# Optimization experiments

Hardware: AMD Instinct MI355X
Metric: run time of the kernel (lower is better)

Reference implementation:

```python
import jax, jax.numpy as jnp
import numpy as np


def setup_inputs() -> dict:
    key = jax.random.key(0)
    kq, kk = jax.random.split(key)
    B, Q, K, D = 32, 512, 512, 1024
    queries = jax.random.normal(kq, (B, Q, D), dtype=jnp.float32)
    keys = jax.random.normal(kk, (B, K, D), dtype=jnp.float32)
    # ProbabilityConverter learned scalars (is_temperature=True, is_bias=True)
    temperature = jnp.ones((), dtype=jnp.float32)
    bias = jnp.zeros((), dtype=jnp.float32)
    return {"queries": queries, "keys": keys, "temperature": temperature, "bias": bias}


def reference(queries, keys, temperature, bias):
    # Dot scoring: (B, Q, D) x (B, K, D) -> (B, Q, K)
    logits = jnp.einsum("bqd,bkd->bqk", queries, keys)
    # keys.eq(0.0)[:, :, :1].transpose(1, 2): mask positions where first key feature == 0
    key_mask = (keys[:, :, 0] == 0.0)[:, None, :]  # (B, 1, K)
    neg_inf = jnp.array(-jnp.inf, dtype=logits.dtype)
    logits = jnp.where(key_mask, neg_inf, logits)
    # confidence = sigmoid((logsumexp(logits) + bias) * temperature)
    approx_max_logit = jax.nn.logsumexp(logits, axis=-1)  # (B, Q)
    confidence = jax.nn.sigmoid((approx_max_logit + bias) * temperature)
    attn = jax.nn.softmax(logits, axis=-1)  # (B, Q, K)
    return attn, confidence
```

## Files before the change

kernel.cpp:

```cpp
#include <hip/hip_runtime.h>
#include <math.h>
#include <stdint.h>


#define NB 32
#define NQ 512
#define NK 512
#define ND 1024
#define BK 32
#define NT (ND / BK)
#define BM1 64
#define BM8 64
#define ASTRIDE 520
#define TILE_BYTES 65536
#define WS_TILES ((size_t)NB * NT * TILE_BYTES)
#define WS_TOTAL (WS_TILES + (size_t)NB * NK * 4)

typedef __attribute__((ext_vector_type(8))) short short8;
typedef __attribute__((ext_vector_type(4))) float f32x4;

__device__ __forceinline__ void bf_split(float x, unsigned& hbits, float& lo) {
  unsigned u = __float_as_uint(x);
  unsigned r = u + 0x7fffu + ((u >> 16) & 1u);
  hbits = r & 0xffff0000u;
  lo = x - __uint_as_float(hbits);
}
__device__ __forceinline__ unsigned pack_rn(float x0, float x1) {
  unsigned u0 = __float_as_uint(x0), u1 = __float_as_uint(x1);
  unsigned r0 = u0 + 0x7fffu + ((u0 >> 16) & 1u);
  unsigned r1 = u1 + 0x7fffu + ((u1 >> 16) & 1u);
  return (r0 >> 16) | (r1 & 0xffff0000u);
}

__device__ __forceinline__ int lds_off_write(int r, int c4) {
  int slot = ((c4 >> 1) + (r >> 1)) & 3;
  return r * 32 + slot * 8 + (c4 & 1) * 4;
}
__device__ __forceinline__ int lds_off_read(int r, int quad) {
  int slot = (quad + (r >> 1)) & 3;
  return r * 32 + slot * 8;
}

__global__ __launch_bounds__(256)
void convert_k(const float* __restrict__ Kg, unsigned char* __restrict__ ws) {
  const int bx = blockIdx.x;
  const int batch = bx >> 5, kt = bx & 31;
  const float* src = Kg + (size_t)batch * NK * ND + kt * BK;
  unsigned short* hiB = (unsigned short*)(ws + (size_t)bx * TILE_BYTES);
  unsigned short* loB = hiB + 32768 / 2;
  float* maskB = (float*)(ws + WS_TILES) + batch * NK;

#pragma unroll
  for (int i = 0; i < 16; ++i) {
    int idx = threadIdx.x + 256 * i;
    int c = idx >> 3, c4 = idx & 7;
    float4 v = *(const float4*)(src + (size_t)c * ND + c4 * 4);
    unsigned h0, h1, h2, h3;
    float l0, l1, l2, l3;
    bf_split(v.x, h0, l0); bf_split(v.y, h1, l1);
    bf_split(v.z, h2, l2); bf_split(v.w, h3, l3);
    int off = c * 32 + c4 * 4;
    *(uint2*)(&hiB[off]) = make_uint2((h0 >> 16) | h1, (h2 >> 16) | h3);
    *(uint2*)(&loB[off]) = make_uint2(pack_rn(l0, l1), pack_rn(l2, l3));
    if (kt == 0 && c4 == 0) maskB[c] = v.x;
  }
}

#define MFMA_BF16 __builtin_amdgcn_mfma_f32_16x16x32_bf16

#define BODY8(KT, CURB, NXTB)                                                  \
  do {                                                                         \
    if ((KT) + 1 < NT) {                                                       \
      const unsigned char* tb = wsB + (size_t)((KT) + 1) * TILE_BYTES;         \
      NXTB[0] = *(const short8*)(tb + boff);                                   \
      NXTB[1] = *(const short8*)(tb + 1024 + boff);                            \
      NXTB[2] = *(const short8*)(tb + 32768 + boff);                           \
      NXTB[3] = *(const short8*)(tb + 32768 + 1024 + boff);                    \
    }                                                                          \
    const int ktL = (KT) & 15;                                                 \
    short8 ahi[4], alo[4];                                                     \
    _Pragma("unroll") for (int mt = 0; mt < 4; ++mt) {                         \
      int off = (mt * 16 + ln15) * ASTRIDE + ktL * 32 + quad * 8;              \
      ahi[mt] = *(const short8*)(&sAhi[off]);                                  \
      alo[mt] = *(const short8*)(&sAlo[off]);                                  \
    }                                                                          \
    _Pragma("unroll") for (int nt = 0; nt < 2; ++nt) {                         \
      _Pragma("unroll") for (int mt = 0; mt < 4; ++mt) {                       \
        acc[mt][nt] = MFMA_BF16(ahi[mt], CURB[nt], acc[mt][nt], 0, 0, 0);      \
        acc[mt][nt] = MFMA_BF16(ahi[mt], CURB[2 + nt], acc[mt][nt], 0, 0, 0);  \
        acc[mt][nt] = MFMA_BF16(alo[mt], CURB[nt], acc[mt][nt], 0, 0, 0);      \
      }                                                                        \
    }                                                                          \
  } while (0)

__global__ __launch_bounds__(1024, 4)
void attn_fused_v8(const float* __restrict__ Qg,
                   const unsigned char* __restrict__ ws,
                   const float* __restrict__ Tp, const float* __restrict__ Bp,
                   float* __restrict__ attn, float* __restrict__ conf) {
  __shared__ __align__(16) unsigned short sAhi[BM8 * ASTRIDE];
  __shared__ __align__(16) unsigned short sAlo[BM8 * ASTRIDE];
  __shared__ __align__(16) float sRedA[BM8][16];
  __shared__ __align__(16) float sRedB[BM8][16];

  const int tid = threadIdx.x;
  const int g = blockIdx.x;
  const int batch = g & 31;
  const int q0 = (g >> 5) * BM8;
  const int ln = tid & 63, w = tid >> 6;
  const int ln15 = ln & 15, quad = ln >> 4;
  const int col0 = w * 32;

  const float* Qp = Qg + ((size_t)batch * NQ + q0) * ND;
  const unsigned char* wsB = ws + (size_t)batch * NT * TILE_BYTES;
  const float* maskB = (const float*)(ws + WS_TILES) + batch * NK;

  const int boff = (col0 << 6) + (ln15 << 6) + (quad << 4);

  f32x4 acc[4][2];
#pragma unroll
  for (int mt = 0; mt < 4; ++mt)
#pragma unroll
    for (int nt = 0; nt < 2; ++nt) acc[mt][nt] = (f32x4){0.f, 0.f, 0.f, 0.f};

  auto stage_half = [&](int h) {
#pragma unroll
    for (int i = 0; i < 4; ++i) {
      int idx = tid + 1024 * i;
      int row = idx >> 6, kc8 = idx & 63;
      const float* p = Qp + (size_t)row * ND + h * 512 + kc8 * 8;
      float4 va = *(const float4*)(p);
      float4 vb = *(const float4*)(p + 4);
      unsigned h0, h1, h2, h3, h4, h5, h6, h7;
      float l0, l1, l2, l3, l4, l5, l6, l7;
      bf_split(va.x, h0, l0); bf_split(va.y, h1, l1);
      bf_split(va.z, h2, l2); bf_split(va.w, h3, l3);
      bf_split(vb.x, h4, l4); bf_split(vb.y, h5, l5);
      bf_split(vb.z, h6, l6); bf_split(vb.w, h7, l7);
      int off = row * ASTRIDE + kc8 * 8;
      *(uint4*)(&sAhi[off]) = make_uint4((h0 >> 16) | h1, (h2 >> 16) | h3,
                                         (h4 >> 16) | h5, (h6 >> 16) | h7);
      *(uint4*)(&sAlo[off]) = make_uint4(pack_rn(l0, l1), pack_rn(l2, l3),
                                         pack_rn(l4, l5), pack_rn(l6, l7));
    }
  };

  stage_half(0);
  short8 pbA[4], pbB[4];
  pbA[0] = *(const short8*)(wsB + boff);
  pbA[1] = *(const short8*)(wsB + 1024 + boff);
  pbA[2] = *(const short8*)(wsB + 32768 + boff);
  pbA[3] = *(const short8*)(wsB + 32768 + 1024 + boff);
  __syncthreads();

#pragma unroll 1
  for (int kt = 0; kt < 16; kt += 2) {
    BODY8(kt, pbA, pbB);
    BODY8(kt + 1, pbB, pbA);
  }

  __syncthreads();
  stage_half(1);
  __syncthreads();

#pragma unroll 1
  for (int kt = 16; kt < 32; kt += 2) {
    BODY8(kt, pbA, pbB);
    BODY8(kt + 1, pbB, pbA);
  }

  const float NEGINF = -__builtin_inff();
  float rm[4][4];
#pragma unroll
  for (int mt = 0; mt < 4; ++mt)
#pragma unroll
    for (int rg = 0; rg < 4; ++rg) rm[mt][rg] = NEGINF;

#pragma unroll
  for (int nt = 0; nt < 2; ++nt) {
    int col = col0 + nt * 16 + ln15;
    bool msk = (maskB[col] == 0.0f);
#pragma unroll
    for (int mt = 0; mt < 4; ++mt)
#pragma unroll
      for (int rg = 0; rg < 4; ++rg) {
        float v = msk ? NEGINF : acc[mt][nt][rg];
        acc[mt][nt][rg] = v;
        rm[mt][rg] = fmaxf(rm[mt][rg], v);
      }
  }
#pragma unroll
  for (int mt = 0; mt < 4; ++mt)
#pragma unroll
    for (int rg = 0; rg < 4; ++rg) {
      float v = rm[mt][rg];
#pragma unroll
      for (int d = 1; d < 16; d <<= 1) v = fmaxf(v, __shfl_xor(v, d, 64));
      rm[mt][rg] = v;
    }
  if (ln15 == 0) {
#pragma unroll
    for (int mt = 0; mt < 4; ++mt)
#pragma unroll
      for (int rg = 0; rg < 4; ++rg)
        sRedA[mt * 16 + quad * 4 + rg][w] = rm[mt][rg];
  }
  __syncthreads();

  float gmax[4][4], gsum[4][4];
#pragma unroll
  for (int mt = 0; mt < 4; ++mt)
#pragma unroll
    for (int rg = 0; rg < 4; ++rg) {
      int row = mt * 16 + quad * 4 + rg;
      f32x4 p0 = *(const f32x4*)(&sRedA[row][0]);
      f32x4 p1 = *(const f32x4*)(&sRedA[row][4]);
      f32x4 p2 = *(const f32x4*)(&sRedA[row][8]);
      f32x4 p3 = *(const f32x4*)(&sRedA[row][12]);
      float m01 = fmaxf(fmaxf(fmaxf(p0[0], p0[1]), fmaxf(p0[2], p0[3])),
                        fmaxf(fmaxf(p1[0], p1[1]), fmaxf(p1[2], p1[3])));
      float m23 = fmaxf(fmaxf(fmaxf(p2[0], p2[1]), fmaxf(p2[2], p2[3])),
                        fmaxf(fmaxf(p3[0], p3[1]), fmaxf(p3[2], p3[3])));
      gmax[mt][rg] = fmaxf(m01, m23);
      gsum[mt][rg] = 0.f;
    }

#pragma unroll
  for (int nt = 0; nt < 2; ++nt)
#pragma unroll
    for (int mt = 0; mt < 4; ++mt)
#pragma unroll
      for (int rg = 0; rg < 4; ++rg) {
        float e = __expf(acc[mt][nt][rg] - gmax[mt][rg]);
        acc[mt][nt][rg] = e;
        gsum[mt][rg] += e;
      }
#pragma unroll
  for (int mt = 0; mt < 4; ++mt)
#pragma unroll
    for (int rg = 0; rg < 4; ++rg) {
      float v = gsum[mt][rg];
#pragma unroll
      for (int d = 1; d < 16; d <<= 1) v += __shfl_xor(v, d, 64);
      gsum[mt][rg] = v;
    }
  if (ln15 == 0) {
#pragma unroll
    for (int mt = 0; mt < 4; ++mt)
#pragma unroll
      for (int rg = 0; rg < 4; ++rg)
        sRedB[mt * 16 + quad * 4 + rg][w] = gsum[mt][rg];
  }
  __syncthreads();
#pragma unroll
  for (int mt = 0; mt < 4; ++mt)
#pragma unroll
    for (int rg = 0; rg < 4; ++rg) {
      int row = mt * 16 + quad * 4 + rg;
      f32x4 p0 = *(const f32x4*)(&sRedB[row][0]);
      f32x4 p1 = *(const f32x4*)(&sRedB[row][4]);
      f32x4 p2 = *(const f32x4*)(&sRedB[row][8]);
      f32x4 p3 = *(const f32x4*)(&sRedB[row][12]);
      gsum[mt][rg] = ((p0[0] + p0[1]) + (p0[2] + p0[3])) +
                     ((p1[0] + p1[1]) + (p1[2] + p1[3])) +
                     ((p2[0] + p2[1]) + (p2[2] + p2[3])) +
                     ((p3[0] + p3[1]) + (p3[2] + p3[3]));
    }

  float* outBase = attn + ((size_t)batch * NQ + q0) * NK;
#pragma unroll
  for (int mt = 0; mt < 4; ++mt)
#pragma unroll
    for (int rg = 0; rg < 4; ++rg) {
      int row = mt * 16 + quad * 4 + rg;
      float inv = 1.0f / gsum[mt][rg];
#pragma unroll
      for (int nt = 0; nt < 2; ++nt)
        outBase[(size_t)row * NK + col0 + nt * 16 + ln15] = acc[mt][nt][rg] * inv;
    }

  if (w == 0 && ln15 == 0) {
    float tv = Tp[0], bv = Bp[0];
#pragma unroll
    for (int mt = 0; mt < 4; ++mt)
#pragma unroll
      for (int rg = 0; rg < 4; ++rg) {
        int row = mt * 16 + quad * 4 + rg;
        float lse = gmax[mt][rg] + __logf(gsum[mt][rg]);
        float t = (lse + bv) * tv;
        conf[(size_t)batch * NQ + q0 + row] = 1.0f / (1.0f + __expf(-t));
      }
  }
}

__global__ __launch_bounds__(256, 1)
void attn_fused_v1(const float* __restrict__ Qg, const float* __restrict__ Kg,
                   const float* __restrict__ Tp, const float* __restrict__ Bp,
                   float* __restrict__ attn, float* __restrict__ conf) {
  __shared__ __align__(16) unsigned short sAhi[BM1 * BK];
  __shared__ __align__(16) unsigned short sAlo[BM1 * BK];
  __shared__ __align__(16) unsigned short sBhi[NK * BK];
  __shared__ __align__(16) unsigned short sBlo[NK * BK];
  __shared__ float sRedA[4][BM1];
  __shared__ float sRedB[4][BM1];

  const int tid = threadIdx.x;
  const int g = blockIdx.x;
  const int batch = g & 31;
  const int q0 = (g >> 5) * BM1;
  const int ln = tid & 63, w = tid >> 6;
  const int ln15 = ln & 15, quad = ln >> 4;
  const int wn0 = w * 128;

  const float* Qp = Qg + ((size_t)batch * NQ + q0) * ND;
  const float* Kp = Kg + (size_t)batch * NK * ND;

  f32x4 acc[4][8];
#pragma unroll
  for (int mt = 0; mt < 4; ++mt)
#pragma unroll
    for (int nt = 0; nt < 8; ++nt) acc[mt][nt] = (f32x4){0.f, 0.f, 0.f, 0.f};

  float4 pb[16], pa[2];
#pragma unroll
  for (int i = 0; i < 16; ++i) {
    int idx = tid + 256 * i, r = idx >> 3, c4 = idx & 7;
    pb[i] = *(const float4*)(Kp + (size_t)r * ND + c4 * 4);
  }
#pragma unroll
  for (int i = 0; i < 2; ++i) {
    int idx = tid + 256 * i, r = idx >> 3, c4 = idx & 7;
    pa[i] = *(const float4*)(Qp + (size_t)r * ND + c4 * 4);
  }

  for (int kt = 0; kt < NT; ++kt) {
    if (kt) __syncthreads();
#pragma unroll
    for (int i = 0; i < 2; ++i) {
      int idx = tid + 256 * i, r = idx >> 3, c4 = idx & 7;
      int off = lds_off_write(r, c4);
      unsigned h0, h1, h2, h3; float l0, l1, l2, l3;
      bf_split(pa[i].x, h0, l0); bf_split(pa[i].y, h1, l1);
      bf_split(pa[i].z, h2, l2); bf_split(pa[i].w, h3, l3);
      *(uint2*)(&sAhi[off]) = make_uint2((h0 >> 16) | h1, (h2 >> 16) | h3);
      *(uint2*)(&sAlo[off]) = make_uint2(pack_rn(l0, l1), pack_rn(l2, l3));
    }
#pragma unroll
    for (int i = 0; i < 16; ++i) {
      int idx = tid + 256 * i, r = idx >> 3, c4 = idx & 7;
      int off = lds_off_write(r, c4);
      unsigned h0, h1, h2, h3; float l0, l1, l2, l3;
      bf_split(pb[i].x, h0, l0); bf_split(pb[i].y, h1, l1);
      bf_split(pb[i].z, h2, l2); bf_split(pb[i].w, h3, l3);
      *(uint2*)(&sBhi[off]) = make_uint2((h0 >> 16) | h1, (h2 >> 16) | h3);
      *(uint2*)(&sBlo[off]) = make_uint2(pack_rn(l0, l1), pack_rn(l2, l3));
    }
    __syncthreads();

    if (kt < NT - 1) {
      const float* Kq = Kp + (kt + 1) * BK;
      const float* Qq = Qp + (kt + 1) * BK;
#pragma unroll
      for (int i = 0; i < 16; ++i) {
        int idx = tid + 256 * i, r = idx >> 3, c4 = idx & 7;
        pb[i] = *(const float4*)(Kq + (size_t)r * ND + c4 * 4);
      }
#pragma unroll
      for (int i = 0; i < 2; ++i) {
        int idx = tid + 256 * i, r = idx >> 3, c4 = idx & 7;
        pa[i] = *(const float4*)(Qq + (size_t)r * ND + c4 * 4);
      }
    }

    short8 ahi[4], alo[4];
#pragma unroll
    for (int mt = 0; mt < 4; ++mt) {
      int off = lds_off_read(mt * 16 + ln15, quad);
      ahi[mt] = *(const short8*)(&sAhi[off]);
      alo[mt] = *(const short8*)(&sAlo[off]);
    }
#pragma unroll
    for (int nt = 0; nt < 8; ++nt) {
      int off = lds_off_read(wn0 + nt * 16 + ln15, quad);
      short8 bhi = *(const short8*)(&sBhi[off]);
      short8 blo = *(const short8*)(&sBlo[off]);
#pragma unroll
      for (int mt = 0; mt < 4; ++mt) {
        acc[mt][nt] = MFMA_BF16(ahi[mt], bhi, acc[mt][nt], 0, 0, 0);
        acc[mt][nt] = MFMA_BF16(ahi[mt], blo, acc[mt][nt], 0, 0, 0);
        acc[mt][nt] = MFMA_BF16(alo[mt], bhi, acc[mt][nt], 0, 0, 0);
      }
    }
  }

  const float NEGINF = -__builtin_inff();
  float rm[4][4];
#pragma unroll
  for (int mt = 0; mt < 4; ++mt)
#pragma unroll
    for (int rg = 0; rg < 4; ++rg) rm[mt][rg] = NEGINF;
#pragma unroll
  for (int nt = 0; nt < 8; ++nt) {
    int col = wn0 + nt * 16 + ln15;
    bool msk = (Kp[(size_t)col * ND] == 0.0f);
#pragma unroll
    for (int mt = 0; mt < 4; ++mt)
#pragma unroll
      for (int rg = 0; rg < 4; ++rg) {
        float v = msk ? NEGINF : acc[mt][nt][rg];
        acc[mt][nt][rg] = v;
        rm[mt][rg] = fmaxf(rm[mt][rg], v);
      }
  }
#pragma unroll
  for (int mt = 0; mt < 4; ++mt)
#pragma unroll
    for (int rg = 0; rg < 4; ++rg) {
      float v = rm[mt][rg];
#pragma unroll
      for (int d = 1; d < 16; d <<= 1) v = fmaxf(v, __shfl_xor(v, d, 64));
      rm[mt][rg] = v;
    }
  if (ln15 == 0)
#pragma unroll
    for (int mt = 0; mt < 4; ++mt)
#pragma unroll
      for (int rg = 0; rg < 4; ++rg)
        sRedA[w][mt * 16 + quad * 4 + rg] = rm[mt][rg];
  __syncthreads();

  float gmax[4][4], gsum[4][4];
#pragma unroll
  for (int mt = 0; mt < 4; ++mt)
#pragma unroll
    for (int rg = 0; rg < 4; ++rg) {
      int row = mt * 16 + quad * 4 + rg;
      gmax[mt][rg] = fmaxf(fmaxf(sRedA[0][row], sRedA[1][row]),
                           fmaxf(sRedA[2][row], sRedA[3][row]));
      gsum[mt][rg] = 0.f;
    }
#pragma unroll
  for (int nt = 0; nt < 8; ++nt)
#pragma unroll
    for (int mt = 0; mt < 4; ++mt)
#pragma unroll
      for (int rg = 0; rg < 4; ++rg) {
        float e = __expf(acc[mt][nt][rg] - gmax[mt][rg]);
        acc[mt][nt][rg] = e;
        gsum[mt][rg] += e;
      }
#pragma unroll
  for (int mt = 0; mt < 4; ++mt)
#pragma unroll
    for (int rg = 0; rg < 4; ++rg) {
      float v = gsum[mt][rg];
#pragma unroll
      for (int d = 1; d < 16; d <<= 1) v += __shfl_xor(v, d, 64);
      gsum[mt][rg] = v;
    }
  if (ln15 == 0)
#pragma unroll
    for (int mt = 0; mt < 4; ++mt)
#pragma unroll
      for (int rg = 0; rg < 4; ++rg)
        sRedB[w][mt * 16 + quad * 4 + rg] = gsum[mt][rg];
  __syncthreads();
#pragma unroll
  for (int mt = 0; mt < 4; ++mt)
#pragma unroll
    for (int rg = 0; rg < 4; ++rg) {
      int row = mt * 16 + quad * 4 + rg;
      gsum[mt][rg] = sRedB[0][row] + sRedB[1][row] + sRedB[2][row] + sRedB[3][row];
    }

  float* outBase = attn + ((size_t)batch * NQ + q0) * NK;
#pragma unroll
  for (int mt = 0; mt < 4; ++mt)
#pragma unroll
    for (int rg = 0; rg < 4; ++rg) {
      int row = mt * 16 + quad * 4 + rg;
      float inv = 1.0f / gsum[mt][rg];
#pragma unroll
      for (int nt = 0; nt < 8; ++nt)
        outBase[(size_t)row * NK + wn0 + nt * 16 + ln15] = acc[mt][nt][rg] * inv;
    }
  if (w == 0 && ln15 == 0) {
    float tv = Tp[0], bv = Bp[0];
#pragma unroll
    for (int mt = 0; mt < 4; ++mt)
#pragma unroll
      for (int rg = 0; rg < 4; ++rg) {
        int row = mt * 16 + quad * 4 + rg;
        float lse = gmax[mt][rg] + __logf(gsum[mt][rg]);
        float t = (lse + bv) * tv;
        conf[(size_t)batch * NQ + q0 + row] = 1.0f / (1.0f + __expf(-t));
      }
  }
}

extern "C" void kernel_launch(void* const* d_in, const int* in_sizes, int n_in,
                              void* d_out, int out_size, void* d_ws, size_t ws_size,
                              hipStream_t stream) {
  const float* q = (const float*)d_in[0];
  const float* k = (const float*)d_in[1];
  const float* temp = (const float*)d_in[2];
  const float* bias = (const float*)d_in[3];
  float* attn = (float*)d_out;
  float* conf = attn + (size_t)NB * NQ * NK;

  if (ws_size >= WS_TOTAL) {
    hipLaunchKernelGGL(convert_k, dim3(NB * NT), dim3(256), 0, stream,
                       k, (unsigned char*)d_ws);
    hipLaunchKernelGGL(attn_fused_v8, dim3(NB * (NQ / BM8)), dim3(1024), 0, stream,
                       q, (const unsigned char*)d_ws, temp, bias, attn, conf);
  } else {
    hipLaunchKernelGGL(attn_fused_v1, dim3(NB * (NQ / BM1)), dim3(256), 0, stream,
                       q, k, temp, bias, attn, conf);
  }
}
```

Before: 218.6 us.

## Fuse K bf16 hi/lo split into main attention kernel, drop convert pass

Removes the separate kernel that pre-split K into bf16 hi/lo tiles in workspace. The fused kernel now loads fp32 K rows directly into registers and splits them in-register before the MFMAs, and reads the mask from K. This eliminates a launch and the workspace write/read round trip. In exchange, every Q-tile block repeats the split arithmetic on K. The small-workspace fallback kernel is deleted.

```diff
diff --git a/kernel.cpp b/kernel.cpp
--- a/kernel.cpp
+++ b/kernel.cpp
@@ -9,15 +9,12 @@
 #define ND 1024
 #define BK 32
 #define NT (ND / BK)
-#define BM1 64
-#define BM8 64
+#define BM9 64
 #define ASTRIDE 520
-#define TILE_BYTES 65536
-#define WS_TILES ((size_t)NB * NT * TILE_BYTES)
-#define WS_TOTAL (WS_TILES + (size_t)NB * NK * 4)
 
 typedef __attribute__((ext_vector_type(8))) short short8;
 typedef __attribute__((ext_vector_type(4))) float f32x4;
+typedef __attribute__((ext_vector_type(4))) unsigned int uint32x4;
 
 __device__ __forceinline__ void bf_split(float x, unsigned& hbits, float& lo) {
   unsigned u = __float_as_uint(x);
@@ -32,50 +29,33 @@
   return (r0 >> 16) | (r1 & 0xffff0000u);
 }
 
-__device__ __forceinline__ int lds_off_write(int r, int c4) {
-  int slot = ((c4 >> 1) + (r >> 1)) & 3;
-  return r * 32 + slot * 8 + (c4 & 1) * 4;
-}
-__device__ __forceinline__ int lds_off_read(int r, int quad) {
-  int slot = (quad + (r >> 1)) & 3;
-  return r * 32 + slot * 8;
-}
-
-__global__ __launch_bounds__(256)
-void convert_k(const float* __restrict__ Kg, unsigned char* __restrict__ ws) {
-  const int bx = blockIdx.x;
-  const int batch = bx >> 5, kt = bx & 31;
-  const float* src = Kg + (size_t)batch * NK * ND + kt * BK;
-  unsigned short* hiB = (unsigned short*)(ws + (size_t)bx * TILE_BYTES);
-  unsigned short* loB = hiB + 32768 / 2;
-  float* maskB = (float*)(ws + WS_TILES) + batch * NK;
-
-#pragma unroll
-  for (int i = 0; i < 16; ++i) {
-    int idx = threadIdx.x + 256 * i;
-    int c = idx >> 3, c4 = idx & 7;
-    float4 v = *(const float4*)(src + (size_t)c * ND + c4 * 4);
-    unsigned h0, h1, h2, h3;
-    float l0, l1, l2, l3;
-    bf_split(v.x, h0, l0); bf_split(v.y, h1, l1);
-    bf_split(v.z, h2, l2); bf_split(v.w, h3, l3);
-    int off = c * 32 + c4 * 4;
-    *(uint2*)(&hiB[off]) = make_uint2((h0 >> 16) | h1, (h2 >> 16) | h3);
-    *(uint2*)(&loB[off]) = make_uint2(pack_rn(l0, l1), pack_rn(l2, l3));
-    if (kt == 0 && c4 == 0) maskB[c] = v.x;
-  }
+__device__ __forceinline__ void split8(const float4& va, const float4& vb,
+                                       short8& hi, short8& lo) {
+  unsigned h0, h1, h2, h3, h4, h5, h6, h7;
+  float l0, l1, l2, l3, l4, l5, l6, l7;
+  bf_split(va.x, h0, l0); bf_split(va.y, h1, l1);
+  bf_split(va.z, h2, l2); bf_split(va.w, h3, l3);
+  bf_split(vb.x, h4, l4); bf_split(vb.y, h5, l5);
+  bf_split(vb.z, h6, l6); bf_split(vb.w, h7, l7);
+  uint32x4 hu = {(h0 >> 16) | h1, (h2 >> 16) | h3,
+                 (h4 >> 16) | h5, (h6 >> 16) | h7};
+  uint32x4 lu = {pack_rn(l0, l1), pack_rn(l2, l3),
+                 pack_rn(l4, l5), pack_rn(l6, l7)};
+  hi = __builtin_bit_cast(short8, hu);
+  lo = __builtin_bit_cast(short8, lu);
 }
 
 #define MFMA_BF16 __builtin_amdgcn_mfma_f32_16x16x32_bf16
 
-#define BODY8(KT, CURB, NXTB)                                                  \
+#define BODY9(KT, CURR, NXTR)                                                  \
   do {                                                                         \
     if ((KT) + 1 < NT) {                                                       \
-      const unsigned char* tb = wsB + (size_t)((KT) + 1) * TILE_BYTES;         \
-      NXTB[0] = *(const short8*)(tb + boff);                                   \
-      NXTB[1] = *(const short8*)(tb + 1024 + boff);                            \
-      NXTB[2] = *(const short8*)(tb + 32768 + boff);                           \
-      NXTB[3] = *(const short8*)(tb + 32768 + 1024 + boff);                    \
+      const float* kp0 = kb0 + ((KT) + 1) * BK;                                \
+      const float* kp1 = kb1 + ((KT) + 1) * BK;                                \
+      NXTR[0] = *(const float4*)(kp0);                                         \
+      NXTR[1] = *(const float4*)(kp0 + 4);                                     \
+      NXTR[2] = *(const float4*)(kp1);                                         \
+      NXTR[3] = *(const float4*)(kp1 + 4);                                     \
     }                                                                          \
     const int ktL = (KT) & 15;                                                 \
     short8 ahi[4], alo[4];                                                     \
@@ -84,38 +64,41 @@
       ahi[mt] = *(const short8*)(&sAhi[off]);                                  \
       alo[mt] = *(const short8*)(&sAlo[off]);                                  \
     }                                                                          \
-    _Pragma("unroll") for (int nt = 0; nt < 2; ++nt) {                         \
-      _Pragma("unroll") for (int mt = 0; mt < 4; ++mt) {                       \
-        acc[mt][nt] = MFMA_BF16(ahi[mt], CURB[nt], acc[mt][nt], 0, 0, 0);      \
-        acc[mt][nt] = MFMA_BF16(ahi[mt], CURB[2 + nt], acc[mt][nt], 0, 0, 0);  \
-        acc[mt][nt] = MFMA_BF16(alo[mt], CURB[nt], acc[mt][nt], 0, 0, 0);      \
-      }                                                                        \
+    short8 bhi0, blo0, bhi1, blo1;                                             \
+    split8(CURR[0], CURR[1], bhi0, blo0);                                      \
+    split8(CURR[2], CURR[3], bhi1, blo1);                                      \
+    _Pragma("unroll") for (int mt = 0; mt < 4; ++mt) {                         \
+      acc[mt][0] = MFMA_BF16(ahi[mt], bhi0, acc[mt][0], 0, 0, 0);              \
+      acc[mt][0] = MFMA_BF16(ahi[mt], blo0, acc[mt][0], 0, 0, 0);              \
+      acc[mt][0] = MFMA_BF16(alo[mt], bhi0, acc[mt][0], 0, 0, 0);              \
+      acc[mt][1] = MFMA_BF16(ahi[mt], bhi1, acc[mt][1], 0, 0, 0);              \
+      acc[mt][1] = MFMA_BF16(ahi[mt], blo1, acc[mt][1], 0, 0, 0);              \
+      acc[mt][1] = MFMA_BF16(alo[mt], bhi1, acc[mt][1], 0, 0, 0);              \
     }                                                                          \
   } while (0)
 
 __global__ __launch_bounds__(1024, 4)
-void attn_fused_v8(const float* __restrict__ Qg,
-                   const unsigned char* __restrict__ ws,
+void attn_fused_v9(const float* __restrict__ Qg, const float* __restrict__ Kg,
                    const float* __restrict__ Tp, const float* __restrict__ Bp,
                    float* __restrict__ attn, float* __restrict__ conf) {
-  __shared__ __align__(16) unsigned short sAhi[BM8 * ASTRIDE];
-  __shared__ __align__(16) unsigned short sAlo[BM8 * ASTRIDE];
-  __shared__ __align__(16) float sRedA[BM8][16];
-  __shared__ __align__(16) float sRedB[BM8][16];
+  __shared__ __align__(16) unsigned short sAhi[BM9 * ASTRIDE];
+  __shared__ __align__(16) unsigned short sAlo[BM9 * ASTRIDE];
+  __shared__ __align__(16) float sRedA[BM9][16];
+  __shared__ __align__(16) float sRedB[BM9][16];
 
   const int tid = threadIdx.x;
   const int g = blockIdx.x;
   const int batch = g & 31;
-  const int q0 = (g >> 5) * BM8;
+  const int q0 = (g >> 5) * BM9;
   const int ln = tid & 63, w = tid >> 6;
   const int ln15 = ln & 15, quad = ln >> 4;
   const int col0 = w * 32;
 
   const float* Qp = Qg + ((size_t)batch * NQ + q0) * ND;
-  const unsigned char* wsB = ws + (size_t)batch * NT * TILE_BYTES;
-  const float* maskB = (const float*)(ws + WS_TILES) + batch * NK;
-
-  const int boff = (col0 << 6) + (ln15 << 6) + (quad << 4);
+  const float* Kp = Kg + (size_t)batch * NK * ND;
+
+  const float* kb0 = Kp + (size_t)(col0 + ln15) * ND + quad * 8;
+  const float* kb1 = kb0 + 16 * ND;
 
   f32x4 acc[4][2];
 #pragma unroll
@@ -146,17 +129,17 @@
   };
 
   stage_half(0);
-  short8 pbA[4], pbB[4];
-  pbA[0] = *(const short8*)(wsB + boff);
-  pbA[1] = *(const short8*)(wsB + 1024 + boff);
-  pbA[2] = *(const short8*)(wsB + 32768 + boff);
-  pbA[3] = *(const short8*)(wsB + 32768 + 1024 + boff);
+  float4 pbA[4], pbB[4];
+  pbA[0] = *(const float4*)(kb0);
+  pbA[1] = *(const float4*)(kb0 + 4);
+  pbA[2] = *(const float4*)(kb1);
+  pbA[3] = *(const float4*)(kb1 + 4);
   __syncthreads();
 
 #pragma unroll 1
   for (int kt = 0; kt < 16; kt += 2) {
-    BODY8(kt, pbA, pbB);
-    BODY8(kt + 1, pbB, pbA);
+    BODY9(kt, pbA, pbB);
+    BODY9(kt + 1, pbB, pbA);
   }
 
   __syncthreads();
@@ -165,8 +148,8 @@
 
 #pragma unroll 1
   for (int kt = 16; kt < 32; kt += 2) {
-    BODY8(kt, pbA, pbB);
-    BODY8(kt + 1, pbB, pbA);
+    BODY9(kt, pbA, pbB);
+    BODY9(kt + 1, pbB, pbA);
   }
 
   const float NEGINF = -__builtin_inff();
@@ -179,7 +162,7 @@
 #pragma unroll
   for (int nt = 0; nt < 2; ++nt) {
     int col = col0 + nt * 16 + ln15;
-    bool msk = (maskB[col] == 0.0f);
+    bool msk = (Kp[(size_t)col * ND] == 0.0f);
 #pragma unroll
     for (int mt = 0; mt < 4; ++mt)
 #pragma unroll
@@ -293,211 +276,6 @@
   }
 }
 
-__global__ __launch_bounds__(256, 1)
-void attn_fused_v1(const float* __restrict__ Qg, const float* __restrict__ Kg,
-                   const float* __restrict__ Tp, const float* __restrict__ Bp,
-                   float* __restrict__ attn, float* __restrict__ conf) {
-  __shared__ __align__(16) unsigned short sAhi[BM1 * BK];
-  __shared__ __align__(16) unsigned short sAlo[BM1 * BK];
-  __shared__ __align__(16) unsigned short sBhi[NK * BK];
-  __shared__ __align__(16) unsigned short sBlo[NK * BK];
-  __shared__ float sRedA[4][BM1];
-  __shared__ float sRedB[4][BM1];
-
-  const int tid = threadIdx.x;
-  const int g = blockIdx.x;
-  const int batch = g & 31;
-  const int q0 = (g >> 5) * BM1;
-  const int ln = tid & 63, w = tid >> 6;
-  const int ln15 = ln & 15, quad = ln >> 4;
-  const int wn0 = w * 128;
-
-  const float* Qp = Qg + ((size_t)batch * NQ + q0) * ND;
-  const float* Kp = Kg + (size_t)batch * NK * ND;
-
-  f32x4 acc[4][8];
-#pragma unroll
-  for (int mt = 0; mt < 4; ++mt)
-#pragma unroll
-    for (int nt = 0; nt < 8; ++nt) acc[mt][nt] = (f32x4){0.f, 0.f, 0.f, 0.f};
-
-  float4 pb[16], pa[2];
-#pragma unroll
-  for (int i = 0; i < 16; ++i) {
-    int idx = tid + 256 * i, r = idx >> 3, c4 = idx & 7;
-    pb[i] = *(const float4*)(Kp + (size_t)r * ND + c4 * 4);
-  }
-#pragma unroll
-  for (int i = 0; i < 2; ++i) {
-    int idx = tid + 256 * i, r = idx >> 3, c4 = idx & 7;
-    pa[i] = *(const float4*)(Qp + (size_t)r * ND + c4 * 4);
-  }
-
-  for (int kt = 0; kt < NT; ++kt) {
-    if (kt) __syncthreads();
-#pragma unroll
-    for (int i = 0; i < 2; ++i) {
-      int idx = tid + 256 * i, r = idx >> 3, c4 = idx & 7;
-      int off = lds_off_write(r, c4);
-      unsigned h0, h1, h2, h3; float l0, l1, l2, l3;
-      bf_split(pa[i].x, h0, l0); bf_split(pa[i].y, h1, l1);
-      bf_split(pa[i].z, h2, l2); bf_split(pa[i].w, h3, l3);
-      *(uint2*)(&sAhi[off]) = make_uint2((h0 >> 16) | h1, (h2 >> 16) | h3);
-      *(uint2*)(&sAlo[off]) = make_uint2(pack_rn(l0, l1), pack_rn(l2, l3));
-    }
-#pragma unroll
-    for (int i = 0; i < 16; ++i) {
-      int idx = tid + 256 * i, r = idx >> 3, c4 = idx & 7;
-      int off = lds_off_write(r, c4);
-      unsigned h0, h1, h2, h3; float l0, l1, l2, l3;
-      bf_split(pb[i].x, h0, l0); bf_split(pb[i].y, h1, l1);
-      bf_split(pb[i].z, h2, l2); bf_split(pb[i].w, h3, l3);
-      *(uint2*)(&sBhi[off]) = make_uint2((h0 >> 16) | h1, (h2 >> 16) | h3);
-      *(uint2*)(&sBlo[off]) = make_uint2(pack_rn(l0, l1), pack_rn(l2, l3));
-    }
-    __syncthreads();
-
-    if (kt < NT - 1) {
-      const float* Kq = Kp + (kt + 1) * BK;
-      const float* Qq = Qp + (kt + 1) * BK;
-#pragma unroll
-      for (int i = 0; i < 16; ++i) {
-        int idx = tid + 256 * i, r = idx >> 3, c4 = idx & 7;
-        pb[i] = *(const float4*)(Kq + (size_t)r * ND + c4 * 4);
-      }
-#pragma unroll
-      for (int i = 0; i < 2; ++i) {
-        int idx = tid + 256 * i, r = idx >> 3, c4 = idx & 7;
-        pa[i] = *(const float4*)(Qq + (size_t)r * ND + c4 * 4);
-      }
-    }
-
-    short8 ahi[4], alo[4];
-#pragma unroll
-    for (int mt = 0; mt < 4; ++mt) {
-      int off = lds_off_read(mt * 16 + ln15, quad);
-      ahi[mt] = *(const short8*)(&sAhi[off]);
-      alo[mt] = *(const short8*)(&sAlo[off]);
-    }
-#pragma unroll
-    for (int nt = 0; nt < 8; ++nt) {
-      int off = lds_off_read(wn0 + nt * 16 + ln15, quad);
-      short8 bhi = *(const short8*)(&sBhi[off]);
-      short8 blo = *(const short8*)(&sBlo[off]);
-#pragma unroll
-      for (int mt = 0; mt < 4; ++mt) {
-        acc[mt][nt] = MFMA_BF16(ahi[mt], bhi, acc[mt][nt], 0, 0, 0);
-        acc[mt][nt] = MFMA_BF16(ahi[mt], blo, acc[mt][nt], 0, 0, 0);
-        acc[mt][nt] = MFMA_BF16(alo[mt], bhi, acc[mt][nt], 0, 0, 0);
-      }
-    }
-  }
-
-  const float NEGINF = -__builtin_inff();
-  float rm[4][4];
-#pragma unroll
-  for (int mt = 0; mt < 4; ++mt)
-#pragma unroll
-    for (int rg = 0; rg < 4; ++rg) rm[mt][rg] = NEGINF;
-#pragma unroll
-  for (int nt = 0; nt < 8; ++nt) {
-    int col = wn0 + nt * 16 + ln15;
-    bool msk = (Kp[(size_t)col * ND] == 0.0f);
-#pragma unroll
-    for (int mt = 0; mt < 4; ++mt)
-#pragma unroll
-      for (int rg = 0; rg < 4; ++rg) {
-        float v = msk ? NEGINF : acc[mt][nt][rg];
-        acc[mt][nt][rg] = v;
-        rm[mt][rg] = fmaxf(rm[mt][rg], v);
-      }
-  }
-#pragma unroll
-  for (int mt = 0; mt < 4; ++mt)
-#pragma unroll
-    for (int rg = 0; rg < 4; ++rg) {
-      float v = rm[mt][rg];
-#pragma unroll
-      for (int d = 1; d < 16; d <<= 1) v = fmaxf(v, __shfl_xor(v, d, 64));
-      rm[mt][rg] = v;
-    }
-  if (ln15 == 0)
-#pragma unroll
-    for (int mt = 0; mt < 4; ++mt)
-#pragma unroll
-      for (int rg = 0; rg < 4; ++rg)
-        sRedA[w][mt * 16 + quad * 4 + rg] = rm[mt][rg];
-  __syncthreads();
-
-  float gmax[4][4], gsum[4][4];
-#pragma unroll
-  for (int mt = 0; mt < 4; ++mt)
-#pragma unroll
-    for (int rg = 0; rg < 4; ++rg) {
-      int row = mt * 16 + quad * 4 + rg;
-      gmax[mt][rg] = fmaxf(fmaxf(sRedA[0][row], sRedA[1][row]),
-                           fmaxf(sRedA[2][row], sRedA[3][row]));
-      gsum[mt][rg] = 0.f;
-    }
-#pragma unroll
-  for (int nt = 0; nt < 8; ++nt)
-#pragma unroll
-    for (int mt = 0; mt < 4; ++mt)
-#pragma unroll
-      for (int rg = 0; rg < 4; ++rg) {
-        float e = __expf(acc[mt][nt][rg] - gmax[mt][rg]);
-        acc[mt][nt][rg] = e;
-        gsum[mt][rg] += e;
-      }
-#pragma unroll
-  for (int mt = 0; mt < 4; ++mt)
-#pragma unroll
-    for (int rg = 0; rg < 4; ++rg) {
-      float v = gsum[mt][rg];
-#pragma unroll
-      for (int d = 1; d < 16; d <<= 1) v += __shfl_xor(v, d, 64);
-      gsum[mt][rg] = v;
-    }
-  if (ln15 == 0)
-#pragma unroll
-    for (int mt = 0; mt < 4; ++mt)
-#pragma unroll
-      for (int rg = 0; rg < 4; ++rg)
-        sRedB[w][mt * 16 + quad * 4 + rg] = gsum[mt][rg];
-  __syncthreads();
-#pragma unroll
-  for (int mt = 0; mt < 4; ++mt)
-#pragma unroll
-    for (int rg = 0; rg < 4; ++rg) {
-      int row = mt * 16 + quad * 4 + rg;
-      gsum[mt][rg] = sRedB[0][row] + sRedB[1][row] + sRedB[2][row] + sRedB[3][row];
-    }
-
-  float* outBase = attn + ((size_t)batch * NQ + q0) * NK;
-#pragma unroll
-  for (int mt = 0; mt < 4; ++mt)
-#pragma unroll
-    for (int rg = 0; rg < 4; ++rg) {
-      int row = mt * 16 + quad * 4 + rg;
-      float inv = 1.0f / gsum[mt][rg];
-#pragma unroll
-      for (int nt = 0; nt < 8; ++nt)
-        outBase[(size_t)row * NK + wn0 + nt * 16 + ln15] = acc[mt][nt][rg] * inv;
-    }
-  if (w == 0 && ln15 == 0) {
-    float tv = Tp[0], bv = Bp[0];
-#pragma unroll
-    for (int mt = 0; mt < 4; ++mt)
-#pragma unroll
-      for (int rg = 0; rg < 4; ++rg) {
-        int row = mt * 16 + quad * 4 + rg;
-        float lse = gmax[mt][rg] + __logf(gsum[mt][rg]);
-        float t = (lse + bv) * tv;
-        conf[(size_t)batch * NQ + q0 + row] = 1.0f / (1.0f + __expf(-t));
-      }
-  }
-}
-
 extern "C" void kernel_launch(void* const* d_in, const int* in_sizes, int n_in,
                               void* d_out, int out_size, void* d_ws, size_t ws_size,
                               hipStream_t stream) {
@@ -508,13 +286,7 @@
   float* attn = (float*)d_out;
   float* conf = attn + (size_t)NB * NQ * NK;
 
-  if (ws_size >= WS_TOTAL) {
-    hipLaunchKernelGGL(convert_k, dim3(NB * NT), dim3(256), 0, stream,
-                       k, (unsigned char*)d_ws);
-    hipLaunchKernelGGL(attn_fused_v8, dim3(NB * (NQ / BM8)), dim3(1024), 0, stream,
-                       q, (const unsigned char*)d_ws, temp, bias, attn, conf);
-  } else {
-    hipLaunchKernelGGL(attn_fused_v1, dim3(NB * (NQ / BM1)), dim3(256), 0, stream,
-                       q, k, temp, bias, attn, conf);
-  }
-}
+  (void)d_ws; (void)ws_size;
+  hipLaunchKernelGGL(attn_fused_v9, dim3(NB * (NQ / BM9)), dim3(1024), 0, stream,
+                     q, k, temp, bias, attn, conf);
+}
```

Measured after the change: 221.6 us. No clear change (+1.4%).

## Split key dimension across blocks with partial softmax and separate combine pass

Applied to the files above, without the earlier changes.

The fused kernel is replaced by a partial kernel where each block covers 128 query rows and half of the keys. It stages Q in four K-quarters and adds a barrier after each MFMA step. Each block writes unnormalized exponentials plus per-half row max and sum to workspace. A new combine kernel then rescales every attention row and computes confidence. The aim is to reuse the key tiles across more query rows and reduce per-block LDS, at the cost of an extra full read and write of the attention output and one more launch.

```diff
diff --git a/kernel.cpp b/kernel.cpp
--- a/kernel.cpp
+++ b/kernel.cpp
@@ -10,11 +10,14 @@
 #define BK 32
 #define NT (ND / BK)
 #define BM1 64
-#define BM8 64
-#define ASTRIDE 520
+#define BMP 128
+#define KHALF 256
+#define AST2 264
 #define TILE_BYTES 65536
 #define WS_TILES ((size_t)NB * NT * TILE_BYTES)
-#define WS_TOTAL (WS_TILES + (size_t)NB * NK * 4)
+#define MASK_BYTES ((size_t)NB * NK * 4)
+#define MS_BYTES ((size_t)NB * NQ * 2 * 4)
+#define WS_TOTAL (WS_TILES + MASK_BYTES + 2 * MS_BYTES)
 
 typedef __attribute__((ext_vector_type(8))) short short8;
 typedef __attribute__((ext_vector_type(4))) float f32x4;
@@ -68,7 +71,7 @@
 
 #define MFMA_BF16 __builtin_amdgcn_mfma_f32_16x16x32_bf16
 
-#define BODY8(KT, CURB, NXTB)                                                  \
+#define BODYP(KT, CURB, NXTB)                                                  \
   do {                                                                         \
     if ((KT) + 1 < NT) {                                                       \
       const unsigned char* tb = wsB + (size_t)((KT) + 1) * TILE_BYTES;         \
@@ -77,10 +80,10 @@
       NXTB[2] = *(const short8*)(tb + 32768 + boff);                           \
       NXTB[3] = *(const short8*)(tb + 32768 + 1024 + boff);                    \
     }                                                                          \
-    const int ktL = (KT) & 15;                                                 \
+    const int ktL = (KT) & 7;                                                  \
     short8 ahi[4], alo[4];                                                     \
     _Pragma("unroll") for (int mt = 0; mt < 4; ++mt) {                         \
-      int off = (mt * 16 + ln15) * ASTRIDE + ktL * 32 + quad * 8;              \
+      int off = (wr * 64 + mt * 16 + ln15) * AST2 + ktL * 32 + quad * 8;       \
       ahi[mt] = *(const short8*)(&sAhi[off]);                                  \
       alo[mt] = *(const short8*)(&sAlo[off]);                                  \
     }                                                                          \
@@ -91,31 +94,33 @@
         acc[mt][nt] = MFMA_BF16(alo[mt], CURB[nt], acc[mt][nt], 0, 0, 0);      \
       }                                                                        \
     }                                                                          \
+    __builtin_amdgcn_s_barrier();                                              \
   } while (0)
 
 __global__ __launch_bounds__(1024, 4)
-void attn_fused_v8(const float* __restrict__ Qg,
-                   const unsigned char* __restrict__ ws,
-                   const float* __restrict__ Tp, const float* __restrict__ Bp,
-                   float* __restrict__ attn, float* __restrict__ conf) {
-  __shared__ __align__(16) unsigned short sAhi[BM8 * ASTRIDE];
-  __shared__ __align__(16) unsigned short sAlo[BM8 * ASTRIDE];
-  __shared__ __align__(16) float sRedA[BM8][16];
-  __shared__ __align__(16) float sRedB[BM8][16];
+void attn_part(const float* __restrict__ Qg, const unsigned char* __restrict__ ws,
+               float* __restrict__ attn, float* __restrict__ Mws,
+               float* __restrict__ Sws) {
+  __shared__ __align__(16) unsigned short sAhi[BMP * AST2];
+  __shared__ __align__(16) unsigned short sAlo[BMP * AST2];
+  __shared__ __align__(16) float sRed[BMP][8];
 
   const int tid = threadIdx.x;
   const int g = blockIdx.x;
-  const int batch = g & 31;
-  const int q0 = (g >> 5) * BM8;
+  const int b = g & 31;
+  const int qh = g >> 5;
+  const int qc = qh >> 1;
+  const int h = qh & 1;
   const int ln = tid & 63, w = tid >> 6;
   const int ln15 = ln & 15, quad = ln >> 4;
-  const int col0 = w * 32;
-
-  const float* Qp = Qg + ((size_t)batch * NQ + q0) * ND;
-  const unsigned char* wsB = ws + (size_t)batch * NT * TILE_BYTES;
-  const float* maskB = (const float*)(ws + WS_TILES) + batch * NK;
-
-  const int boff = (col0 << 6) + (ln15 << 6) + (quad << 4);
+  const int wr = w >> 3, wc = w & 7;
+  const int col0 = wc * 32;
+
+  const float* Qp = Qg + ((size_t)b * NQ + qc * BMP) * ND;
+  const unsigned char* wsB = ws + (size_t)b * NT * TILE_BYTES;
+  const float* maskB = (const float*)(ws + WS_TILES) + b * NK;
+
+  const int boff = ((h * KHALF + col0 + ln15) << 6) + (quad << 4);
 
   f32x4 acc[4][2];
 #pragma unroll
@@ -123,12 +128,12 @@
 #pragma unroll
     for (int nt = 0; nt < 2; ++nt) acc[mt][nt] = (f32x4){0.f, 0.f, 0.f, 0.f};
 
-  auto stage_half = [&](int h) {
+  auto stage_quarter = [&](int kq) {
 #pragma unroll
     for (int i = 0; i < 4; ++i) {
       int idx = tid + 1024 * i;
-      int row = idx >> 6, kc8 = idx & 63;
-      const float* p = Qp + (size_t)row * ND + h * 512 + kc8 * 8;
+      int row = idx >> 5, kc8 = idx & 31;
+      const float* p = Qp + (size_t)row * ND + kq * 256 + kc8 * 8;
       float4 va = *(const float4*)(p);
       float4 vb = *(const float4*)(p + 4);
       unsigned h0, h1, h2, h3, h4, h5, h6, h7;
@@ -137,7 +142,7 @@
       bf_split(va.z, h2, l2); bf_split(va.w, h3, l3);
       bf_split(vb.x, h4, l4); bf_split(vb.y, h5, l5);
       bf_split(vb.z, h6, l6); bf_split(vb.w, h7, l7);
-      int off = row * ASTRIDE + kc8 * 8;
+      int off = row * AST2 + kc8 * 8;
       *(uint4*)(&sAhi[off]) = make_uint4((h0 >> 16) | h1, (h2 >> 16) | h3,
                                          (h4 >> 16) | h5, (h6 >> 16) | h7);
       *(uint4*)(&sAlo[off]) = make_uint4(pack_rn(l0, l1), pack_rn(l2, l3),
@@ -145,7 +150,7 @@
     }
   };
 
-  stage_half(0);
+  stage_quarter(0);
   short8 pbA[4], pbB[4];
   pbA[0] = *(const short8*)(wsB + boff);
   pbA[1] = *(const short8*)(wsB + 1024 + boff);
@@ -154,19 +159,21 @@
   __syncthreads();
 
 #pragma unroll 1
-  for (int kt = 0; kt < 16; kt += 2) {
-    BODY8(kt, pbA, pbB);
-    BODY8(kt + 1, pbB, pbA);
-  }
-
-  __syncthreads();
-  stage_half(1);
-  __syncthreads();
-
-#pragma unroll 1
-  for (int kt = 16; kt < 32; kt += 2) {
-    BODY8(kt, pbA, pbB);
-    BODY8(kt + 1, pbB, pbA);
+  for (int kq = 0; kq < 4; ++kq) {
+    if (kq) {
+      __syncthreads();
+      stage_quarter(kq);
+      __syncthreads();
+    }
+    const int k0 = kq * 8;
+    BODYP(k0 + 0, pbA, pbB);
+    BODYP(k0 + 1, pbB, pbA);
+    BODYP(k0 + 2, pbA, pbB);
+    BODYP(k0 + 3, pbB, pbA);
+    BODYP(k0 + 4, pbA, pbB);
+    BODYP(k0 + 5, pbB, pbA);
+    BODYP(k0 + 6, pbA, pbB);
+    BODYP(k0 + 7, pbB, pbA);
   }
 
   const float NEGINF = -__builtin_inff();
@@ -178,7 +185,7 @@
 
 #pragma unroll
   for (int nt = 0; nt < 2; ++nt) {
-    int col = col0 + nt * 16 + ln15;
+    int col = h * KHALF + col0 + nt * 16 + ln15;
     bool msk = (maskB[col] == 0.0f);
 #pragma unroll
     for (int mt = 0; mt < 4; ++mt)
@@ -203,7 +210,7 @@
     for (int mt = 0; mt < 4; ++mt)
 #pragma unroll
       for (int rg = 0; rg < 4; ++rg)
-        sRedA[mt * 16 + quad * 4 + rg][w] = rm[mt][rg];
+        sRed[wr * 64 + mt * 16 + quad * 4 + rg][wc] = rm[mt][rg];
   }
   __syncthreads();
 
@@ -212,16 +219,11 @@
   for (int mt = 0; mt < 4; ++mt)
 #pragma unroll
     for (int rg = 0; rg < 4; ++rg) {
-      int row = mt * 16 + quad * 4 + rg;
-      f32x4 p0 = *(const f32x4*)(&sRedA[row][0]);
-      f32x4 p1 = *(const f32x4*)(&sRedA[row][4]);
-      f32x4 p2 = *(const f32x4*)(&sRedA[row][8]);
-      f32x4 p3 = *(const f32x4*)(&sRedA[row][12]);
-      float m01 = fmaxf(fmaxf(fmaxf(p0[0], p0[1]), fmaxf(p0[2], p0[3])),
-                        fmaxf(fmaxf(p1[0], p1[1]), fmaxf(p1[2], p1[3])));
-      float m23 = fmaxf(fmaxf(fmaxf(p2[0], p2[1]), fmaxf(p2[2], p2[3])),
-                        fmaxf(fmaxf(p3[0], p3[1]), fmaxf(p3[2], p3[3])));
-      gmax[mt][rg] = fmaxf(m01, m23);
+      int row = wr * 64 + mt * 16 + quad * 4 + rg;
+      f32x4 p0 = *(const f32x4*)(&sRed[row][0]);
+      f32x4 p1 = *(const f32x4*)(&sRed[row][4]);
+      gmax[mt][rg] = fmaxf(fmaxf(fmaxf(p0[0], p0[1]), fmaxf(p0[2], p0[3])),
+                           fmaxf(fmaxf(p1[0], p1[1]), fmaxf(p1[2], p1[3])));
       gsum[mt][rg] = 0.f;
     }
 
@@ -231,7 +233,8 @@
     for (int mt = 0; mt < 4; ++mt)
 #pragma unroll
       for (int rg = 0; rg < 4; ++rg) {
-        float e = __expf(acc[mt][nt][rg] - gmax[mt][rg]);
+        float mu = (gmax[mt][rg] == NEGINF) ? 0.f : gmax[mt][rg];
+        float e = __expf(acc[mt][nt][rg] - mu);
         acc[mt][nt][rg] = e;
         gsum[mt][rg] += e;
       }
@@ -244,52 +247,85 @@
       for (int d = 1; d < 16; d <<= 1) v += __shfl_xor(v, d, 64);
       gsum[mt][rg] = v;
     }
+  __syncthreads();
   if (ln15 == 0) {
 #pragma unroll
     for (int mt = 0; mt < 4; ++mt)
 #pragma unroll
       for (int rg = 0; rg < 4; ++rg)
-        sRedB[mt * 16 + quad * 4 + rg][w] = gsum[mt][rg];
+        sRed[wr * 64 + mt * 16 + quad * 4 + rg][wc] = gsum[mt][rg];
   }
   __syncthreads();
 #pragma unroll
   for (int mt = 0; mt < 4; ++mt)
 #pragma unroll
     for (int rg = 0; rg < 4; ++rg) {
-      int row = mt * 16 + quad * 4 + rg;
-      f32x4 p0 = *(const f32x4*)(&sRedB[row][0]);
-      f32x4 p1 = *(const f32x4*)(&sRedB[row][4]);
-      f32x4 p2 = *(const f32x4*)(&sRedB[row][8]);
-      f32x4 p3 = *(const f32x4*)(&sRedB[row][12]);
+      int row = wr * 64 + mt * 16 + quad * 4 + rg;
+      f32x4 p0 = *(const f32x4*)(&sRed[row][0]);
+      f32x4 p1 = *(const f32x4*)(&sRed[row][4]);
       gsum[mt][rg] = ((p0[0] + p0[1]) + (p0[2] + p0[3])) +
-                     ((p1[0] + p1[1]) + (p1[2] + p1[3])) +
-                     ((p2[0] + p2[1]) + (p2[2] + p2[3])) +
-                     ((p3[0] + p3[1]) + (p3[2] + p3[3]));
-    }
-
-  float* outBase = attn + ((size_t)batch * NQ + q0) * NK;
-#pragma unroll
-  for (int mt = 0; mt < 4; ++mt)
-#pragma unroll
-    for (int rg = 0; rg < 4; ++rg) {
-      int row = mt * 16 + quad * 4 + rg;
-      float inv = 1.0f / gsum[mt][rg];
+                     ((p1[0] + p1[1]) + (p1[2] + p1[3]));
+    }
+
+  float* outBase = attn + ((size_t)b * NQ + qc * BMP) * NK + h * KHALF;
+#pragma unroll
+  for (int mt = 0; mt < 4; ++mt)
+#pragma unroll
+    for (int rg = 0; rg < 4; ++rg) {
+      int row = wr * 64 + mt * 16 + quad * 4 + rg;
 #pragma unroll
       for (int nt = 0; nt < 2; ++nt)
-        outBase[(size_t)row * NK + col0 + nt * 16 + ln15] = acc[mt][nt][rg] * inv;
-    }
-
-  if (w == 0 && ln15 == 0) {
-    float tv = Tp[0], bv = Bp[0];
+        outBase[(size_t)row * NK + col0 + nt * 16 + ln15] = acc[mt][nt][rg];
+    }
+
+  if (wc == 0 && ln15 == 0) {
 #pragma unroll
     for (int mt = 0; mt < 4; ++mt)
 #pragma unroll
       for (int rg = 0; rg < 4; ++rg) {
-        int row = mt * 16 + quad * 4 + rg;
-        float lse = gmax[mt][rg] + __logf(gsum[mt][rg]);
-        float t = (lse + bv) * tv;
-        conf[(size_t)batch * NQ + q0 + row] = 1.0f / (1.0f + __expf(-t));
-      }
+        int row = wr * 64 + mt * 16 + quad * 4 + rg;
+        size_t R = (size_t)b * NQ + qc * BMP + row;
+        Mws[R * 2 + h] = gmax[mt][rg];
+        Sws[R * 2 + h] = gsum[mt][rg];
+      }
+  }
+}
+
+__global__ __launch_bounds__(256)
+void combine(float* __restrict__ attn, const float* __restrict__ Mws,
+             const float* __restrict__ Sws, const float* __restrict__ Tp,
+             const float* __restrict__ Bp, float* __restrict__ conf) {
+  const int tid = threadIdx.x;
+  const int ln = tid & 63;
+  const size_t R = (size_t)blockIdx.x * 4 + (tid >> 6);
+
+  float m0 = Mws[R * 2], m1 = Mws[R * 2 + 1];
+  float s0 = Sws[R * 2], s1 = Sws[R * 2 + 1];
+  const float NEGINF = -__builtin_inff();
+  float M = fmaxf(m0, m1);
+  float sc0 = 0.f, sc1 = 0.f, lse = NEGINF;
+  if (M > NEGINF) {
+    float f0 = __expf(m0 - M);
+    float f1 = __expf(m1 - M);
+    float S = s0 * f0 + s1 * f1;
+    float inv = (S > 0.f) ? 1.0f / S : 0.f;
+    sc0 = f0 * inv;
+    sc1 = f1 * inv;
+    lse = M + __logf(S);
+  }
+
+  float* row = attn + R * NK;
+  float sc = (ln < 32) ? sc0 : sc1;
+  f32x4 v0 = *(const f32x4*)(row + ln * 8);
+  f32x4 v1 = *(const f32x4*)(row + ln * 8 + 4);
+  v0 *= sc;
+  v1 *= sc;
+  *(f32x4*)(row + ln * 8) = v0;
+  *(f32x4*)(row + ln * 8 + 4) = v1;
+
+  if (ln == 0) {
+    float t = (lse + Bp[0]) * Tp[0];
+    conf[R] = 1.0f / (1.0f + __expf(-t));
   }
 }
 
@@ -509,10 +545,15 @@
   float* conf = attn + (size_t)NB * NQ * NK;
 
   if (ws_size >= WS_TOTAL) {
+    unsigned char* ws = (unsigned char*)d_ws;
+    float* Mws = (float*)(ws + WS_TILES + MASK_BYTES);
+    float* Sws = (float*)(ws + WS_TILES + MASK_BYTES + MS_BYTES);
     hipLaunchKernelGGL(convert_k, dim3(NB * NT), dim3(256), 0, stream,
-                       k, (unsigned char*)d_ws);
-    hipLaunchKernelGGL(attn_fused_v8, dim3(NB * (NQ / BM8)), dim3(1024), 0, stream,
-                       q, (const unsigned char*)d_ws, temp, bias, attn, conf);
+                       k, ws);
+    hipLaunchKernelGGL(attn_part, dim3(NB * (NQ / BMP) * 2), dim3(1024), 0,
+                       stream, q, ws, attn, Mws, Sws);
+    hipLaunchKernelGGL(combine, dim3(NB * NQ / 4), dim3(256), 0, stream,
+                       attn, Mws, Sws, temp, bias, conf);
   } else {
     hipLaunchKernelGGL(attn_fused_v1, dim3(NB * (NQ / BM1)), dim3(256), 0, stream,
                        q, k, temp, bias, attn, conf);
```

Result: slower. 235.7 us (+7.8%).
